# Kernel tuning notes

Measured on AMD Instinct MI355X. Metric: run time of the kernel, lower is better.

Reference implementation:

```python
import jax, jax.numpy as jnp
import numpy as np
from jax import lax

KH, KW = 9, 9
FC_DIM = 1024
C_RED = FC_DIM // 8  # 128
EPS = 1e-5


def conv_bn_relu(x, w, gamma, beta):
    # 3x3 conv, stride 1, pad 1 (NCHW / OIHW), then batch-stat BN + ReLU
    y = lax.conv_general_dilated(x, w, (1, 1), ((1, 1), (1, 1)),
                                 dimension_numbers=('NCHW', 'OIHW', 'NCHW'))
    mean = y.mean(axis=(0, 2, 3))
    var = y.var(axis=(0, 2, 3))
    y = (y - mean[None, :, None, None]) * lax.rsqrt(var + EPS)[None, :, None, None]
    y = y * gamma[None, :, None, None] + beta[None, :, None, None]
    return jnp.maximum(y, 0.0)


def local_weighting(feat, atten, kH, kW):
    # feat: [B,C,H,W]; atten: [B,H,W,kH*kW]
    # out[b,c,h,w] = sum_k atten[b,h,w,k] * feat_padded[b,c,h+dh_k,w+dw_k]
    B, C, H, W = feat.shape
    ph, pw = kH // 2, kW // 2
    fp = jnp.pad(feat, ((0, 0), (0, 0), (ph, ph), (pw, pw)))
    out = jnp.zeros_like(feat)
    k = 0
    for dh in range(kH):
        for dw in range(kW):
            out = out + fp[:, :, dh:dh + H, dw:dw + W] * atten[:, None, :, :, k]
            k += 1
    return out


def setup_inputs() -> dict:
    key = jax.random.key(0)
    ks = jax.random.split(key, 12)
    B, H, W = 4, 64, 64
    sc1 = 1.0 / np.sqrt(FC_DIM * 9)
    sc5 = 1.0 / np.sqrt(C_RED * 9)
    return {
        'low_key': jax.random.normal(ks[0], (B, FC_DIM, H, W), jnp.float32),
        'low_nonkey': jax.random.normal(ks[1], (B, FC_DIM, H, W), jnp.float32),
        'local_atten': jax.random.uniform(ks[2], (B, H, W, KH * KW), jnp.float32),
        'w1': jax.random.normal(ks[3], (C_RED, FC_DIM, 3, 3), jnp.float32) * sc1,
        'g1': jnp.ones((C_RED,), jnp.float32),
        'b1': jnp.zeros((C_RED,), jnp.float32),
        'w4': jax.random.normal(ks[4], (C_RED, FC_DIM, 3, 3), jnp.float32) * sc1,
        'g4': jnp.ones((C_RED,), jnp.float32),
        'b4': jnp.zeros((C_RED,), jnp.float32),
        'w5': jax.random.normal(ks[5], (C_RED, C_RED, 3, 3), jnp.float32) * sc5,
        'g5': jnp.ones((C_RED,), jnp.float32),
        'b5': jnp.zeros((C_RED,), jnp.float32),
        'fc1_w': jax.random.normal(ks[6], (10, C_RED), jnp.float32) * (1.0 / np.sqrt(C_RED)),
        'fc1_b': jnp.zeros((10,), jnp.float32),
        'fc2_w': jax.random.normal(ks[7], (1, 10), jnp.float32) * (1.0 / np.sqrt(10.0)),
        'fc2_b': jnp.zeros((1,), jnp.float32),
    }


def reference(low_key, low_nonkey, local_atten,
              w1, g1, b1, w4, g4, b4, w5, g5, b5,
              fc1_w, fc1_b, fc2_w, fc2_b):
    lk = conv_bn_relu(low_key, w1, g1, b1)          # [B,128,H,W]
    trans = local_weighting(lk, local_atten, KH, KW)
    lnk = conv_bn_relu(low_nonkey, w4, g4, b4)
    out = trans - lnk
    out = conv_bn_relu(out, w5, g5, b5)
    out = out.mean(axis=(2, 3))                      # adaptive avg pool to 1x1 -> [B,128]
    out = out @ fc1_w.T + fc1_b
    out = out @ fc2_w.T + fc2_b                      # [B,1]
    return out
```

## Files before the change

### kernel.cpp

```cpp
#include <hip/hip_runtime.h>
#include <hip/hip_bf16.h>


#define B_ 4
#define CM_ 128

typedef __attribute__((ext_vector_type(8))) short short8;
typedef __attribute__((ext_vector_type(4))) float floatx4;
typedef __attribute__((address_space(3))) unsigned lds_as;
typedef __attribute__((address_space(1))) const unsigned glb_as;

__device__ inline short f2bf(float f) {
  union { float f; unsigned u; } v; v.f = f;
  unsigned r = v.u + 0x7fff + ((v.u >> 16) & 1);
  return (short)(r >> 16);
}
__device__ inline float bf2f(unsigned short u) {
  union { unsigned u; float f; } v; v.u = ((unsigned)u) << 16;
  return v.f;
}

template <int KB>
__global__ void xprep_kernel(const float* __restrict__ x, short* __restrict__ xt) {
  int kb = blockIdx.x >> 4, rg = blockIdx.x & 15;
  int b = blockIdx.y;
  int row = rg * 4 + (threadIdx.x >> 6);
  int col = threadIdx.x & 63;
  const float* xs = x + (((size_t)b * (KB * 32) + kb * 32) * 64 + row) * 64 + col;
  short* xd = xt + ((((size_t)b * KB + kb) * 64 + row) * 64 + col) * 32;
  int sw = (col >> 1) & 3;
#pragma unroll
  for (int u = 0; u < 4; u++) {
    short8 pk;
#pragma unroll
    for (int j = 0; j < 8; j++) pk[j] = f2bf(xs[(size_t)(u * 8 + j) * 4096]);
    *(short8*)(xd + (u ^ sw) * 8) = pk;
  }
}

__global__ void prep1_kernel(const float* __restrict__ x1,
                             const float* __restrict__ w1, const float* __restrict__ w4,
                             const float* __restrict__ w5, const float* __restrict__ atten,
                             short* __restrict__ xt, short* __restrict__ wf1,
                             short* __restrict__ wf4, short* __restrict__ wf5,
                             float* __restrict__ att_t, float* __restrict__ yz) {
  __shared__ float tile[5184];
  int bx = blockIdx.x, tid = threadIdx.x;
  if (bx < 2048) {
    int b = bx & 3, t = bx >> 2;
    int kb = t >> 4, rg = t & 15;
    int row = rg * 4 + (tid >> 6), col = tid & 63;
    const float* xs = x1 + (((size_t)b * 1024 + kb * 32) * 64 + row) * 64 + col;
    short* xd = xt + ((((size_t)b * 32 + kb) * 64 + row) * 64 + col) * 32;
    int sw = (col >> 1) & 3;
#pragma unroll
    for (int u = 0; u < 4; u++) {
      short8 pk;
#pragma unroll
      for (int j = 0; j < 8; j++) pk[j] = f2bf(xs[(size_t)(u * 8 + j) * 4096]);
      *(short8*)(xd + (u ^ sw) * 8) = pk;
    }
    return;
  }
  bx -= 2048;
  if (bx < 1024) {
    const float* w = bx < 512 ? w1 : w4;
    short* wf = bx < 512 ? wf1 : wf4;
    int idx = (bx & 511) * 256 + tid;
    int oc = idx >> 10, ic = idx & 1023;
    int kb = ic >> 5, icb = ic & 31, quad = icb >> 3, j = icb & 7;
    int m = oc >> 4, n16 = oc & 15, lane = quad * 16 + n16;
    const float* wp = w + ((size_t)oc * 1024 + ic) * 9;
    short* base = wf + (size_t)kb * 36864 + lane * 8 + j;
#pragma unroll
    for (int r = 0; r < 3; r++)
#pragma unroll
      for (int s = 0; s < 3; s++)
        base[(size_t)r * 12288 + (s * 8 + m) * 512] = f2bf(wp[r * 3 + s]);
    return;
  }
  bx -= 1024;
  if (bx < 64) {
    int idx = bx * 256 + tid;
    int oc = idx >> 7, ic = idx & 127;
    int kb = ic >> 5, icb = ic & 31, quad = icb >> 3, j = icb & 7;
    int m = oc >> 4, n16 = oc & 15, lane = quad * 16 + n16;
    const float* wp = w5 + ((size_t)oc * 128 + ic) * 9;
    short* base = wf5 + (size_t)kb * 36864 + lane * 8 + j;
#pragma unroll
    for (int r = 0; r < 3; r++)
#pragma unroll
      for (int s = 0; s < 3; s++)
        base[(size_t)r * 12288 + (s * 8 + m) * 512] = f2bf(wp[r * 3 + s]);
    return;
  }
  bx -= 64;
  if (bx < 256) {
    int b = bx >> 6;
    int p0 = (bx & 63) * 64;
    const float* src = atten + ((size_t)b * 4096 + p0) * 81;
    for (int e = tid; e < 5184; e += 256) tile[e] = src[e];
    __syncthreads();
    for (int f = tid; f < 5184; f += 256) {
      int k = f >> 6, w_ = f & 63;
      att_t[((size_t)b * 81 + k) * 4096 + p0 + w_] = tile[w_ * 81 + k];
    }
    return;
  }
  bx -= 256;
  ((float4*)yz)[(size_t)bx * 256 + tid] = make_float4(0.f, 0.f, 0.f, 0.f);
}

template <int KQ, bool ATOMIC>
__global__ __launch_bounds__(256, 3)
void convm_kernel(const short* __restrict__ xt, const short* __restrict__ wf,
                  float* __restrict__ yo, int KBtot) {
  __shared__ __attribute__((aligned(16))) short smem[24576];
  short* sw = smem;
  short* sx = smem + 8192;
  int tid = threadIdx.x, lane = tid & 63, wv = tid >> 6;
  int n16 = lane & 15, quad = lane >> 4;
  int pg = blockIdx.x;
  int b = pg >> 5, h0 = (pg & 31) * 2;
  int kb0 = blockIdx.y * KQ;
  int mh = wv & 1, nh = wv >> 1;

  if (h0 == 0)
    for (int i = tid; i < 1024; i += 256) { ((int*)sx)[i] = 0; ((int*)(sx + 8192))[i] = 0; }
  if (h0 == 62)
    for (int i = tid; i < 1024; i += 256) {
      ((int*)(sx + 3 * 2048))[i] = 0;
      ((int*)(sx + 8192 + 3 * 2048))[i] = 0;
    }

  auto dma_x = [&](int kbr) {
    int row = h0 - 1 + wv;
    if (row >= 0 && row < 64) {
      const short* src =
          xt + ((((size_t)b * KBtot + kb0 + kbr) * 64 + row) * 64) * 32 + lane * 8;
      short* dst = sx + (kbr & 1) * 8192 + wv * 2048 + lane * 8;
#pragma unroll
      for (int t = 0; t < 4; t++)
        __builtin_amdgcn_global_load_lds((glb_as*)(src + t * 512), (lds_as*)(dst + t * 512),
                                         16, 0, 0);
    }
  };
  auto dma_w = [&](int step) {
    const short* src = wf + ((size_t)(kb0 * 9 + step)) * 4096 + wv * 1024 + lane * 8;
    short* dst = sw + (step & 1) * 4096 + wv * 1024 + lane * 8;
#pragma unroll
    for (int t = 0; t < 2; t++)
      __builtin_amdgcn_global_load_lds((glb_as*)(src + t * 512), (lds_as*)(dst + t * 512),
                                       16, 0, 0);
  };

  floatx4 acc[4][4];
#pragma unroll
  for (int i = 0; i < 4; i++)
#pragma unroll
    for (int n = 0; n < 4; n++) acc[i][n] = (floatx4){0.f, 0.f, 0.f, 0.f};

  dma_x(0);
  dma_w(0);
  const int NS = KQ * 9;
  for (int kb = 0; kb < KQ; kb++) {
#pragma unroll
    for (int rs = 0; rs < 9; rs++) {
      int s = kb * 9 + rs;
      __syncthreads();
      if (s + 1 < NS) dma_w(s + 1);
      if (rs == 0 && kb + 1 < KQ) dma_x(kb + 1);
      int r = rs / 3, sp = rs % 3;
      const short* swb = sw + (s & 1) * 4096;
      const short* sxr = sx + (kb & 1) * 8192 + (nh + r) * 2048;
      short8 a[4];
#pragma unroll
      for (int i = 0; i < 4; i++)
        a[i] = *(const short8*)(swb + ((mh * 4 + i) * 64 + lane) * 8);
#pragma unroll
      for (int n = 0; n < 4; n++) {
        int c = n * 16 + n16 + sp - 1;
        int cc = c < 0 ? 0 : (c > 63 ? 63 : c);
        short8 bf = *(const short8*)(sxr + cc * 32 + (quad ^ ((cc >> 1) & 3)) * 8);
        if ((n == 0 && sp == 0) || (n == 3 && sp == 2)) {
          short8 zz = {0, 0, 0, 0, 0, 0, 0, 0};
          bf = (c != cc) ? zz : bf;
        }
#pragma unroll
        for (int i = 0; i < 4; i++)
          acc[i][n] = __builtin_amdgcn_mfma_f32_16x16x32_bf16(a[i], bf, acc[i][n], 0, 0, 0);
      }
    }
  }

  int row = h0 + nh;
#pragma unroll
  for (int i = 0; i < 4; i++)
#pragma unroll
    for (int n = 0; n < 4; n++)
#pragma unroll
      for (int rg = 0; rg < 4; rg++) {
        int oc = mh * 64 + i * 16 + quad * 4 + rg;
        size_t gi = (((size_t)b * CM_ + oc) * 64 + row) * 64 + n * 16 + n16;
        if (ATOMIC)
          atomicAdd(&yo[gi], acc[i][n][rg]);
        else
          yo[gi] = acc[i][n][rg];
      }
}

__global__ void bnstats2_kernel(const float* __restrict__ y1, const float* __restrict__ g1,
                                const float* __restrict__ b1, float2* __restrict__ s1,
                                const float* __restrict__ y4, const float* __restrict__ g4,
                                const float* __restrict__ b4, float2* __restrict__ s4) {
  const float* y = blockIdx.y ? y4 : y1;
  const float* g = blockIdx.y ? g4 : g1;
  const float* bt = blockIdx.y ? b4 : b1;
  float2* scsh = blockIdx.y ? s4 : s1;
  int c = blockIdx.x;
  int tid = threadIdx.x;
  float s = 0.f, s2 = 0.f;
  for (int b = 0; b < B_; b++) {
    const float4* p = (const float4*)(y + ((size_t)(b * CM_) + c) * 4096);
    for (int i = tid; i < 1024; i += 256) {
      float4 v = p[i];
      s += v.x + v.y + v.z + v.w;
      s2 += v.x * v.x + v.y * v.y + v.z * v.z + v.w * v.w;
    }
  }
  for (int off = 32; off > 0; off >>= 1) {
    s += __shfl_down(s, off);
    s2 += __shfl_down(s2, off);
  }
  __shared__ float rs[4], rq[4];
  if ((tid & 63) == 0) { rs[tid >> 6] = s; rq[tid >> 6] = s2; }
  __syncthreads();
  if (tid == 0) {
    float S = rs[0] + rs[1] + rs[2] + rs[3];
    float Q = rq[0] + rq[1] + rq[2] + rq[3];
    float mean = S * (1.f / 16384.f);
    float var = Q * (1.f / 16384.f) - mean * mean;
    float sc = g[c] * rsqrtf(var + 1e-5f);
    scsh[c] = make_float2(sc, bt[c] - mean * sc);
  }
}

__global__ void bnstats_kernel(const float* __restrict__ y, const float* __restrict__ g,
                               const float* __restrict__ bt, float2* __restrict__ scsh) {
  int c = blockIdx.x;
  int tid = threadIdx.x;
  float s = 0.f, s2 = 0.f;
  for (int b = 0; b < B_; b++) {
    const float4* p = (const float4*)(y + ((size_t)(b * CM_) + c) * 4096);
    for (int i = tid; i < 1024; i += 256) {
      float4 v = p[i];
      s += v.x + v.y + v.z + v.w;
      s2 += v.x * v.x + v.y * v.y + v.z * v.z + v.w * v.w;
    }
  }
  for (int off = 32; off > 0; off >>= 1) {
    s += __shfl_down(s, off);
    s2 += __shfl_down(s2, off);
  }
  __shared__ float rs[4], rq[4];
  if ((tid & 63) == 0) { rs[tid >> 6] = s; rq[tid >> 6] = s2; }
  __syncthreads();
  if (tid == 0) {
    float S = rs[0] + rs[1] + rs[2] + rs[3];
    float Q = rq[0] + rq[1] + rq[2] + rq[3];
    float mean = S * (1.f / 16384.f);
    float var = Q * (1.f / 16384.f) - mean * mean;
    float sc = g[c] * rsqrtf(var + 1e-5f);
    scsh[c] = make_float2(sc, bt[c] - mean * sc);
  }
}

__global__ __launch_bounds__(256, 2)
void localw_kernel(const float* __restrict__ y1, const float2* __restrict__ scsh1,
                   const float* __restrict__ y4, const float2* __restrict__ scsh4,
                   const float* __restrict__ att_t, short* __restrict__ xt5,
                   float* __restrict__ y5z) {
  __shared__ unsigned short lkb[16][12][72];
  int bx = blockIdx.x;
  int b = bx >> 4, h0 = (bx & 15) * 4;
  int cg = blockIdx.y;
  int tid = threadIdx.x;
  int lane = tid & 63;
  int wv = tid >> 6;

  {
    float4* z = (float4*)y5z;
    int bid = cg * 64 + bx;
#pragma unroll
    for (int t = 0; t < 4; t++)
      z[(size_t)bid * 1024 + t * 256 + tid] = make_float4(0.f, 0.f, 0.f, 0.f);
  }

  for (int e = tid; e < 16 * 12 * 72; e += 256) {
    int c_l = e / (12 * 72);
    int rem = e % (12 * 72);
    int gri = rem / 72, j = rem % 72;
    int row = h0 - 4 + gri, col = j - 4;
    float v = 0.f;
    if (row >= 0 && row < 64 && col >= 0 && col < 64) {
      float2 ss = scsh1[cg * 16 + c_l];
      v = fmaxf(0.f, y1[((size_t)(b * CM_) + cg * 16 + c_l) * 4096 + row * 64 + col] * ss.x + ss.y);
    }
    lkb[c_l][gri][j] = (unsigned short)f2bf(v);
  }
  __syncthreads();

  float acc[4][4];
#pragma unroll
  for (int cc = 0; cc < 4; cc++)
#pragma unroll
    for (int h_i = 0; h_i < 4; h_i++) acc[cc][h_i] = 0.f;

  const float* ab = att_t + (size_t)b * 81 * 4096 + h0 * 64 + lane;

#pragma unroll
  for (int gri = 0; gri < 12; ++gri) {
    float win[4][9];
#pragma unroll
    for (int cc = 0; cc < 4; ++cc)
#pragma unroll
      for (int dw = 0; dw < 9; ++dw)
        win[cc][dw] = bf2f(lkb[wv * 4 + cc][gri][lane + dw]);
#pragma unroll
    for (int h_i = 0; h_i < 4; ++h_i) {
      int r = gri - h_i;
      if (r < 0 || r > 8) continue;
      const float* ap = ab + (size_t)(r * 9) * 4096 + h_i * 64;
      float a[9];
#pragma unroll
      for (int dw = 0; dw < 9; ++dw) a[dw] = ap[(size_t)dw * 4096];
#pragma unroll
      for (int cc = 0; cc < 4; ++cc)
#pragma unroll
        for (int dw = 0; dw < 9; ++dw)
          acc[cc][h_i] = fmaf(a[dw], win[cc][dw], acc[cc][h_i]);
    }
  }

#pragma unroll
  for (int cc = 0; cc < 4; ++cc) {
    int c = cg * 16 + wv * 4 + cc;
    float2 ss4 = scsh4[c];
    int icb = c & 31;
    int uu = (icb >> 3) ^ ((lane >> 1) & 3);
#pragma unroll
    for (int h_i = 0; h_i < 4; ++h_i) {
      int h = h0 + h_i;
      size_t gi = ((size_t)(b * CM_) + c) * 4096 + h * 64 + lane;
      float lnk = fmaxf(0.f, y4[gi] * ss4.x + ss4.y);
      float dv = acc[cc][h_i] - lnk;
      xt5[((((size_t)b * 4 + (c >> 5)) * 64 + h) * 64 + lane) * 32 + uu * 8 + (icb & 7)] =
          f2bf(dv);
    }
  }
}

__global__ void pool_kernel(const float* __restrict__ y, const float2* __restrict__ scsh,
                            float* __restrict__ pooled) {
  int bc = blockIdx.x;
  int c = bc & 127;
  float2 ss = scsh[c];
  const float4* p = (const float4*)(y + (size_t)bc * 4096);
  float s = 0.f;
  for (int i = threadIdx.x; i < 1024; i += 256) {
    float4 v = p[i];
    s += fmaxf(0.f, v.x * ss.x + ss.y) + fmaxf(0.f, v.y * ss.x + ss.y) +
         fmaxf(0.f, v.z * ss.x + ss.y) + fmaxf(0.f, v.w * ss.x + ss.y);
  }
  for (int off = 32; off > 0; off >>= 1) s += __shfl_down(s, off);
  __shared__ float rs[4];
  if ((threadIdx.x & 63) == 0) rs[threadIdx.x >> 6] = s;
  __syncthreads();
  if (threadIdx.x == 0) pooled[bc] = (rs[0] + rs[1] + rs[2] + rs[3]) * (1.f / 4096.f);
}

__global__ void fc_kernel(const float* __restrict__ pooled, const float* __restrict__ fc1w,
                          const float* __restrict__ fc1b, const float* __restrict__ fc2w,
                          const float* __restrict__ fc2b, float* __restrict__ out) {
  int lane = threadIdx.x;
  float p[B_][10];
#pragma unroll
  for (int b = 0; b < B_; b++)
#pragma unroll
    for (int j = 0; j < 10; j++) p[b][j] = 0.f;
  for (int c = lane; c < CM_; c += 64) {
#pragma unroll
    for (int b = 0; b < B_; b++) {
      float pv = pooled[b * CM_ + c];
#pragma unroll
      for (int j = 0; j < 10; j++) p[b][j] = fmaf(pv, fc1w[j * CM_ + c], p[b][j]);
    }
  }
  for (int off = 32; off > 0; off >>= 1)
#pragma unroll
    for (int b = 0; b < B_; b++)
#pragma unroll
      for (int j = 0; j < 10; j++) p[b][j] += __shfl_down(p[b][j], off);
  if (lane == 0) {
    for (int b = 0; b < B_; b++) {
      float o = fc2b[0];
      for (int j = 0; j < 10; j++) o += fc2w[j] * (p[b][j] + fc1b[j]);
      out[b] = o;
    }
  }
}

extern "C" void kernel_launch(void* const* d_in, const int* in_sizes, int n_in,
                              void* d_out, int out_size, void* d_ws, size_t ws_size,
                              hipStream_t stream) {
  const float* low_key    = (const float*)d_in[0];
  const float* low_nonkey = (const float*)d_in[1];
  const float* atten      = (const float*)d_in[2];
  const float* w1  = (const float*)d_in[3];
  const float* g1  = (const float*)d_in[4];
  const float* b1  = (const float*)d_in[5];
  const float* w4  = (const float*)d_in[6];
  const float* g4  = (const float*)d_in[7];
  const float* b4  = (const float*)d_in[8];
  const float* w5  = (const float*)d_in[9];
  const float* g5  = (const float*)d_in[10];
  const float* b5  = (const float*)d_in[11];
  const float* fc1w = (const float*)d_in[12];
  const float* fc1b = (const float*)d_in[13];
  const float* fc2w = (const float*)d_in[14];
  const float* fc2b = (const float*)d_in[15];

  char* w8 = (char*)d_ws;
  short* wf1   = (short*)w8;
  short* wf4   = (short*)(w8 + 2359296);
  short* wf5   = (short*)(w8 + 4718592);
  float* att_t = (float*)(w8 + 5308416);
  short* xt    = (short*)(w8 + 10616832);
  float* y1    = (float*)(w8 + 44171264);
  float* y4    = (float*)(w8 + 52559872);
  float2* scsh1 = (float2*)(w8 + 60948480);
  float2* scsh4 = scsh1 + CM_;
  float2* scsh5 = scsh4 + CM_;
  float* pooled = (float*)(scsh5 + CM_);
  short* xt5 = xt;
  float* y5  = (float*)(w8 + 10616832 + 8388608);
  float* out = (float*)d_out;

  prep1_kernel<<<7488, 256, 0, stream>>>(low_key, w1, w4, w5, atten,
                                         xt, wf1, wf4, wf5, att_t, y1);
  convm_kernel<4, true><<<dim3(128, 8), 256, 0, stream>>>(xt, wf1, y1, 32);
  xprep_kernel<32><<<dim3(512, 4), 256, 0, stream>>>(low_nonkey, xt);
  convm_kernel<4, true><<<dim3(128, 8), 256, 0, stream>>>(xt, wf4, y4, 32);
  bnstats2_kernel<<<dim3(128, 2), 256, 0, stream>>>(y1, g1, b1, scsh1, y4, g4, b4, scsh4);
  localw_kernel<<<dim3(64, 8), 256, 0, stream>>>(y1, scsh1, y4, scsh4, att_t, xt5, y5);
  convm_kernel<1, true><<<dim3(128, 4), 256, 0, stream>>>(xt5, wf5, y5, 4);
  bnstats_kernel<<<128, 256, 0, stream>>>(y5, g5, b5, scsh5);
  pool_kernel<<<512, 256, 0, stream>>>(y5, scsh5, pooled);
  fc_kernel<<<1, 64, 0, stream>>>(pooled, fc1w, fc1b, fc2w, fc2b, out);
}
```

Measured before the change: 441.3 us.

## Load activation tiles directly from global into registers, stage weights per kernel row

The conv kernel stops staging input activation rows in LDS. Each wave now reads its B-operand fragments straight from global memory into registers, with zero masking for out-of-range rows and columns. Weight staging changes from one 3x3 tap per step to a full kernel row of three taps per step, which cuts the number of barriers per channel block from nine to three. The tradeoff is more global traffic and latency exposure for the activation reads, since neighbouring waves and horizontal shifts re-read overlapping data, plus higher register pressure from holding twelve B fragments.

```diff
diff --git a/kernel.cpp b/kernel.cpp
--- a/kernel.cpp
+++ b/kernel.cpp
@@ -115,9 +115,7 @@
 __global__ __launch_bounds__(256, 3)
 void convm_kernel(const short* __restrict__ xt, const short* __restrict__ wf,
                   float* __restrict__ yo, int KBtot) {
-  __shared__ __attribute__((aligned(16))) short smem[24576];
-  short* sw = smem;
-  short* sx = smem + 8192;
+  __shared__ __attribute__((aligned(16))) short sw[24576];
   int tid = threadIdx.x, lane = tid & 63, wv = tid >> 6;
   int n16 = lane & 15, quad = lane >> 4;
   int pg = blockIdx.x;
@@ -125,31 +123,11 @@
   int kb0 = blockIdx.y * KQ;
   int mh = wv & 1, nh = wv >> 1;
 
-  if (h0 == 0)
-    for (int i = tid; i < 1024; i += 256) { ((int*)sx)[i] = 0; ((int*)(sx + 8192))[i] = 0; }
-  if (h0 == 62)
-    for (int i = tid; i < 1024; i += 256) {
-      ((int*)(sx + 3 * 2048))[i] = 0;
-      ((int*)(sx + 8192 + 3 * 2048))[i] = 0;
-    }
-
-  auto dma_x = [&](int kbr) {
-    int row = h0 - 1 + wv;
-    if (row >= 0 && row < 64) {
-      const short* src =
-          xt + ((((size_t)b * KBtot + kb0 + kbr) * 64 + row) * 64) * 32 + lane * 8;
-      short* dst = sx + (kbr & 1) * 8192 + wv * 2048 + lane * 8;
-#pragma unroll
-      for (int t = 0; t < 4; t++)
-        __builtin_amdgcn_global_load_lds((glb_as*)(src + t * 512), (lds_as*)(dst + t * 512),
-                                         16, 0, 0);
-    }
-  };
   auto dma_w = [&](int step) {
-    const short* src = wf + ((size_t)(kb0 * 9 + step)) * 4096 + wv * 1024 + lane * 8;
-    short* dst = sw + (step & 1) * 4096 + wv * 1024 + lane * 8;
-#pragma unroll
-    for (int t = 0; t < 2; t++)
+    const short* src = wf + ((size_t)(kb0 * 3 + step)) * 12288 + wv * 3072 + lane * 8;
+    short* dst = sw + (step & 1) * 12288 + wv * 3072 + lane * 8;
+#pragma unroll
+    for (int t = 0; t < 6; t++)
       __builtin_amdgcn_global_load_lds((glb_as*)(src + t * 512), (lds_as*)(dst + t * 512),
                                        16, 0, 0);
   };
@@ -160,35 +138,42 @@
 #pragma unroll
     for (int n = 0; n < 4; n++) acc[i][n] = (floatx4){0.f, 0.f, 0.f, 0.f};
 
-  dma_x(0);
+  const short8 zz = {0, 0, 0, 0, 0, 0, 0, 0};
   dma_w(0);
-  const int NS = KQ * 9;
+  const int NS = KQ * 3;
   for (int kb = 0; kb < KQ; kb++) {
-#pragma unroll
-    for (int rs = 0; rs < 9; rs++) {
-      int s = kb * 9 + rs;
+    const short* xkb = xt + (((size_t)b * KBtot + kb0 + kb) << 17);
+#pragma unroll
+    for (int r = 0; r < 3; r++) {
+      int s = kb * 3 + r;
       __syncthreads();
+      int row = h0 + nh + r - 1;
+      bool rok = (row >= 0 && row < 64);
+      const short* xr = xkb + (size_t)(rok ? row : 0) * 2048;
+      short8 bf[3][4];
+#pragma unroll
+      for (int sp = 0; sp < 3; sp++)
+#pragma unroll
+        for (int n = 0; n < 4; n++) {
+          int c = n * 16 + n16 + sp - 1;
+          int cc = c < 0 ? 0 : (c > 63 ? 63 : c);
+          short8 v = *(const short8*)(xr + cc * 32 + (quad ^ ((cc >> 1) & 3)) * 8);
+          bf[sp][n] = (rok && c == cc) ? v : zz;
+        }
       if (s + 1 < NS) dma_w(s + 1);
-      if (rs == 0 && kb + 1 < KQ) dma_x(kb + 1);
-      int r = rs / 3, sp = rs % 3;
-      const short* swb = sw + (s & 1) * 4096;
-      const short* sxr = sx + (kb & 1) * 8192 + (nh + r) * 2048;
-      short8 a[4];
-#pragma unroll
-      for (int i = 0; i < 4; i++)
-        a[i] = *(const short8*)(swb + ((mh * 4 + i) * 64 + lane) * 8);
-#pragma unroll
-      for (int n = 0; n < 4; n++) {
-        int c = n * 16 + n16 + sp - 1;
-        int cc = c < 0 ? 0 : (c > 63 ? 63 : c);
-        short8 bf = *(const short8*)(sxr + cc * 32 + (quad ^ ((cc >> 1) & 3)) * 8);
-        if ((n == 0 && sp == 0) || (n == 3 && sp == 2)) {
-          short8 zz = {0, 0, 0, 0, 0, 0, 0, 0};
-          bf = (c != cc) ? zz : bf;
-        }
+      const short* swb = sw + (s & 1) * 12288;
+#pragma unroll
+      for (int sp = 0; sp < 3; sp++) {
+        short8 a[4];
 #pragma unroll
         for (int i = 0; i < 4; i++)
-          acc[i][n] = __builtin_amdgcn_mfma_f32_16x16x32_bf16(a[i], bf, acc[i][n], 0, 0, 0);
+          a[i] = *(const short8*)(swb + ((sp * 8 + mh * 4 + i) * 64 + lane) * 8);
+#pragma unroll
+        for (int n = 0; n < 4; n++)
+#pragma unroll
+          for (int i = 0; i < 4; i++)
+            acc[i][n] =
+                __builtin_amdgcn_mfma_f32_16x16x32_bf16(a[i], bf[sp][n], acc[i][n], 0, 0, 0);
       }
     }
   }
```

After: 520.1 us. 1.18x slower.
